# Kernel optimization log

Measured on AMD Instinct MI355X. Metric: run time of the kernel, lower is better.

Reference implementation:

```python
import jax, jax.numpy as jnp
import numpy as np

N = 8192
IN_F = 256
OUT_F = 128
ALPHA = 0.2  # LeakyReLU negative slope
NEG = -1e12


def setup_inputs() -> dict:
    key = jax.random.key(0)
    k1, k2, k3, k4, k5, k6 = jax.random.split(key, 6)
    inp = jax.random.normal(k1, (N, IN_F), dtype=jnp.float32)
    adj = jax.random.randint(k2, (N, N), 0, 2, dtype=jnp.int32)
    # xavier_uniform with gain=1.414
    def xavier(k, shape, gain=1.414):
        fan_in, fan_out = shape[0], shape[1]
        bound = gain * np.sqrt(6.0 / (fan_in + fan_out))
        return jax.random.uniform(k, shape, jnp.float32, -bound, bound)
    W = xavier(k3, (IN_F, OUT_F))
    a = xavier(k4, (2 * OUT_F, 1))
    W_2 = xavier(k5, (IN_F, OUT_F))
    a_2 = xavier(k6, (2 * OUT_F, 1))
    return {"inp": inp, "adj": adj, "W": W, "a": a, "W_2": W_2, "a_2": a_2}


def _gat_head(h, a_vec, mask):
    # Equivalent to e[i,j] = leakyrelu(a^T [h_i ; h_j]) without N^2*2F concat:
    # split a into source/destination halves.
    a_src = a_vec[:OUT_F, 0]   # [F]
    a_dst = a_vec[OUT_F:, 0]   # [F]
    e = (h @ a_src)[:, None] + (h @ a_dst)[None, :]        # [N, N]
    e = jnp.where(e > 0, e, ALPHA * e)                      # LeakyReLU
    e = jnp.where(mask, e, NEG)
    att = jax.nn.softmax(e, axis=1)                         # [N, N]
    # dropout omitted (eval mode, training=False)
    return att @ h                                          # [N, F]


def reference(inp, adj, W, a, W_2, a_2):
    h = inp @ W      # [N, F]
    h_2 = inp @ W_2  # [N, F]
    mask = adj > 0   # adj is nonneg ints so adj*adj>0 is the same mask
    h_prime = _gat_head(h, a, mask)
    h_prime_2 = _gat_head(h_2, a_2, mask)
    h_total = h_prime + 0.5 * h_prime_2
    return jax.nn.elu(h_total)  # concat=True
```

## Files before the change

kernel.cpp:

```cpp
#include <hip/hip_runtime.h>
#include <hip/hip_fp16.h>

#define NN 8192
#define INF 256
#define OUTF 128
#define LOG2E 1.44269504088896340736f

typedef float f32x4 __attribute__((ext_vector_type(4)));
typedef float f32x16 __attribute__((ext_vector_type(16)));
typedef __fp16 h16x8 __attribute__((ext_vector_type(8)));
typedef __fp16 h16x4 __attribute__((ext_vector_type(4)));
typedef __fp16 h16x2 __attribute__((ext_vector_type(2)));
typedef int i32x4 __attribute__((ext_vector_type(4)));

__device__ __forceinline__ void gload_lds16(const void* g, void* l) {
  __builtin_amdgcn_global_load_lds(
      (const __attribute__((address_space(1))) unsigned int*)g,
      (__attribute__((address_space(3))) unsigned int*)l, 16, 0, 0);
}

__device__ __forceinline__ unsigned encf(float f) {
  int b = __float_as_int(f);
  return b >= 0 ? ((unsigned)b | 0x80000000u) : ~(unsigned)b;
}
__device__ __forceinline__ float decf(unsigned u) {
  int b = (u & 0x80000000u) ? (int)(u & 0x7FFFFFFFu) : ~(int)u;
  return __int_as_float(b);
}

__global__ __launch_bounds__(256) void k0_wt(const float* __restrict__ W1,
                                             const float* __restrict__ W2,
                                             __fp16* __restrict__ WT,
                                             unsigned* __restrict__ GMu) {
  if (blockIdx.x == 0 && threadIdx.x < 2) GMu[threadIdx.x] = 0u;
  int m = blockIdx.x * 256 + threadIdx.x;
  int h = m >> 12;
  int r = m & 4095;
  int c = r >> 5;
  int kb = (r >> 1) & 15;
  int hh = r & 1;
  const float* W = h ? W2 : W1;
  float v[8];
#pragma unroll
  for (int s = 0; s < 8; ++s) {
    int koff = 4 * hh + (s & 3) + 8 * (s >> 2);
    v[s] = W[(kb * 16 + koff) * OUTF + c];
  }
  union { h16x2 h2[4]; i32x4 q; } u;
  u.h2[0] = __builtin_amdgcn_cvt_pkrtz(v[0], v[1]);
  u.h2[1] = __builtin_amdgcn_cvt_pkrtz(v[2], v[3]);
  u.h2[2] = __builtin_amdgcn_cvt_pkrtz(v[4], v[5]);
  u.h2[3] = __builtin_amdgcn_cvt_pkrtz(v[6], v[7]);
  *(i32x4*)(WT + (size_t)h * 32768 + c * 256 + kb * 16 + hh * 8) = u.q;
}

__global__ __launch_bounds__(128) void k1_h(
    const float* __restrict__ inp, const __fp16* __restrict__ WT,
    const float* __restrict__ a1, const float* __restrict__ a2,
    __fp16* __restrict__ hT2, float* __restrict__ S, float* __restrict__ D,
    unsigned* __restrict__ GMu) {
  __shared__ __align__(16) float hl[2][32][136];
  int tid = threadIdx.x;
  int w = tid >> 6;
  int l = tid & 63;
  int lr = l & 31, g = l >> 5;
  int i0 = blockIdx.x * 32;
  const __fp16* WTh = WT + (size_t)w * 32768;
  f32x16 acc[4];
#pragma unroll
  for (int nf = 0; nf < 4; ++nf)
#pragma unroll
    for (int e = 0; e < 16; ++e) acc[nf][e] = 0.0f;
  const float* ip = inp + (size_t)(i0 + lr) * INF;
#pragma unroll
  for (int kb = 0; kb < 16; ++kb) {
    f32x4 q0 = *(const f32x4*)(ip + kb * 16 + 4 * g);
    f32x4 q1 = *(const f32x4*)(ip + kb * 16 + 8 + 4 * g);
    union { h16x2 h2[4]; h16x8 h8; } ua;
    ua.h2[0] = __builtin_amdgcn_cvt_pkrtz(q0[0], q0[1]);
    ua.h2[1] = __builtin_amdgcn_cvt_pkrtz(q0[2], q0[3]);
    ua.h2[2] = __builtin_amdgcn_cvt_pkrtz(q1[0], q1[1]);
    ua.h2[3] = __builtin_amdgcn_cvt_pkrtz(q1[2], q1[3]);
#pragma unroll
    for (int nf = 0; nf < 4; ++nf) {
      h16x8 b = *(const h16x8*)(WTh + (nf * 32 + lr) * 256 + kb * 16 + g * 8);
      acc[nf] = __builtin_amdgcn_mfma_f32_32x32x16_f16(ua.h8, b, acc[nf], 0, 0, 0);
    }
  }
#pragma unroll
  for (int nf = 0; nf < 4; ++nf)
#pragma unroll
    for (int r = 0; r < 16; ++r) {
      int row = (r & 3) + 8 * (r >> 2) + 4 * g;
      hl[w][row][nf * 32 + lr] = acc[nf][r];
    }
  __syncthreads();
  const float* av = w ? a2 : a1;
  float s = 0.f, d = 0.f;
#pragma unroll
  for (int cc = 0; cc < 64; cc += 4) {
    int c = g * 64 + cc;
    f32x4 hv = *(const f32x4*)&hl[w][lr][c];
    f32x4 as = *(const f32x4*)(av + c);
    f32x4 ad = *(const f32x4*)(av + 128 + c);
    s += hv[0] * as[0] + hv[1] * as[1] + hv[2] * as[2] + hv[3] * as[3];
    d += hv[0] * ad[0] + hv[1] * ad[1] + hv[2] * ad[2] + hv[3] * ad[3];
  }
  s += __shfl_xor(s, 32);
  d += __shfl_xor(d, 32);
  float dl = d * LOG2E;
  if (g == 0) {
    S[(size_t)w * NN + i0 + lr] = s * LOG2E;
    D[(size_t)w * NN + i0 + lr] = dl;
  }
  float dmax = dl;
#pragma unroll
  for (int off = 1; off < 32; off <<= 1) dmax = fmaxf(dmax, __shfl_xor(dmax, off));
  if (l == 0) atomicMax(GMu + w, encf(dmax));
  __fp16* hTh = hT2 + (size_t)w * (NN * OUTF);
#pragma unroll
  for (int it = 0; it < 8; ++it) {
    int id = it * 64 + l;
    int jb = id >> 8;
    int sub = id & 255;
    int nf = sub >> 6, lq = sub & 63;
    int lqr = lq & 31, lqg = lq >> 5;
    float v[8];
#pragma unroll
    for (int s2 = 0; s2 < 8; ++s2) {
      int kloc = 4 * lqg + (s2 & 3) + 8 * (s2 >> 2);
      v[s2] = hl[w][jb * 16 + kloc][nf * 32 + lqr];
    }
    union { h16x2 h2[4]; i32x4 q; } u2;
    u2.h2[0] = __builtin_amdgcn_cvt_pkrtz(v[0], v[1]);
    u2.h2[1] = __builtin_amdgcn_cvt_pkrtz(v[2], v[3]);
    u2.h2[2] = __builtin_amdgcn_cvt_pkrtz(v[4], v[5]);
    u2.h2[3] = __builtin_amdgcn_cvt_pkrtz(v[6], v[7]);
    *(i32x4*)(hTh + (size_t)((i0 >> 4) + jb) * 2048 + sub * 8) = u2.q;
  }
}

__global__ __launch_bounds__(256, 2) void k2_attn(
    const int* __restrict__ adj, const __fp16* __restrict__ hT2,
    const float* __restrict__ S, const float* __restrict__ D,
    const unsigned* __restrict__ GMu, __fp16* __restrict__ NUM,
    float* __restrict__ DEN) {
  __shared__ __align__(16) char smem[32768];
  __shared__ __align__(16) char maskL[10240];
  int tid = threadIdx.x;
  int w = tid >> 6;
  int l = tid & 63;
  int lr = l & 31, g2 = l >> 5;
  int h = w >> 1, rq = w & 1;
  int rb = blockIdx.x >> 3, js = blockIdx.x & 7;
  int i0 = rb * 128;
  int jwin = js * 1024;
  int base = i0 + rq * 64;
  int row0 = base + lr, row1 = base + 32 + lr;
  float gm = decf(GMu[h]);
  float sf0 = S[(size_t)h * NN + row0];
  float sf1 = S[(size_t)h * NN + row1];
  float t0 = sf0 + gm, t1 = sf1 + gm;
  float cn0 = -fmaxf(t0, 0.2f * t0) - 1000.0f;
  float cn1 = -fmaxf(t1, 0.2f * t1) - 1000.0f;
  float Ac0 = sf0 + cn0, Bc0 = 0.2f * sf0 + cn0;
  float Ac1 = sf1 + cn1, Bc1 = 0.2f * sf1 + cn1;
  const float* Dh = D + (size_t)h * NN + jwin + 4 * g2;

  f32x16 acc[2][4];
#pragma unroll
  for (int f = 0; f < 2; ++f)
#pragma unroll
    for (int nf = 0; nf < 4; ++nf)
#pragma unroll
      for (int e = 0; e < 16; ++e) acc[f][nf][e] = 0.0f;
  float dsum0 = 0.f, dsum1 = 0.f;

  auto STAGE = [&](int jstep, int b) {
#pragma unroll
    for (int q = 0; q < 4; ++q) {
      int kk_l = q >> 1, hh = q & 1;
      const __fp16* gs = hT2 + (size_t)hh * (NN * OUTF) +
                         (size_t)(js * 64 + jstep * 2 + kk_l) * 2048 + tid * 8;
      gload_lds16(gs, smem + b * 16384 + q * 4096 + tid * 16);
    }
  };

  struct Chunk { i32x4 v0, v1, v2, v3; };
  auto LOADC = [&](int c, Chunk& R) {
    int u = c & 7, gg = c >> 3;
    const int* ab = adj + (size_t)(i0 + w * 32 + u * 4) * NN + jwin + gg * 256 + l * 4;
    R.v0 = *(const i32x4*)(ab);
    R.v1 = *(const i32x4*)(ab + NN);
    R.v2 = *(const i32x4*)(ab + 2 * NN);
    R.v3 = *(const i32x4*)(ab + 3 * NN);
  };
  auto BALLOT = [&](int c, const Chunk& R) {
    int u = c & 7, gg = c >> 3;
    char* mrow = maskL + (gg & 1) * 5120 + (w * 32 + u * 4) * 40 + l * 8;
#pragma unroll
    for (int rr = 0; rr < 4; ++rr) {
      i32x4 vv = rr == 0 ? R.v0 : rr == 1 ? R.v1 : rr == 2 ? R.v2 : R.v3;
      unsigned long long b0 = __ballot(vv[0] != 0);
      unsigned long long b1 = __ballot(vv[1] != 0);
      unsigned long long b2 = __ballot(vv[2] != 0);
      unsigned long long b3 = __ballot(vv[3] != 0);
      unsigned long long bsel = b0;
      bsel = (l == 1) ? b1 : bsel;
      bsel = (l == 2) ? b2 : bsel;
      bsel = (l == 3) ? b3 : bsel;
      if (l < 4) *(unsigned long long*)(mrow + rr * 40) = bsel;
    }
  };

  auto MASK32 = [&](int slot, int r, int u) -> unsigned {
    const unsigned char* mb = (const unsigned char*)(maskL + slot * 5120 + r * 40 + u);
    unsigned m0 = mb[0], m1 = mb[8], m2 = mb[16], m3 = mb[24];
    return m0 | (m1 << 8) | (m2 << 16) | (m3 << 24);
  };

  const h16x2 ones = {(__fp16)1.0f, (__fp16)1.0f};
  h16x8 P[2][2];

  auto SOFTMAX = [&](int jstep, int slot, int u) {
    unsigned bts0 = MASK32(slot, rq * 64 + lr, u) >> g2;
    unsigned bts1 = MASK32(slot, rq * 64 + 32 + lr, u) >> g2;
#pragma unroll
    for (int kk = 0; kk < 2; ++kk) {
      int kkg = jstep * 2 + kk;
      f32x4 d0 = *(const f32x4*)(Dh + kkg * 16);
      f32x4 d1 = *(const f32x4*)(Dh + kkg * 16 + 8);
#pragma unroll
      for (int f = 0; f < 2; ++f) {
        float Af = f ? Ac1 : Ac0, Bf_ = f ? Bc1 : Bc0;
        unsigned bts = f ? bts1 : bts0;
        float pv[8];
#pragma unroll
        for (int s = 0; s < 8; ++s) {
          float dd = (s < 4) ? d0[s] : d1[s - 4];
          const int bitp = 8 * (s & 3) + 4 * kk + 2 * (s >> 2);
          float uu = fmaxf(Af + dd, fmaf(0.2f, dd, Bf_));
          float bfv = (float)((bts >> bitp) & 1u);
          pv[s] = __builtin_amdgcn_exp2f(fmaf(bfv, 1000.0f, uu));
        }
        union { h16x2 h2[4]; h16x8 h8; } uq;
        uq.h2[0] = __builtin_amdgcn_cvt_pkrtz(pv[0], pv[1]);
        uq.h2[1] = __builtin_amdgcn_cvt_pkrtz(pv[2], pv[3]);
        uq.h2[2] = __builtin_amdgcn_cvt_pkrtz(pv[4], pv[5]);
        uq.h2[3] = __builtin_amdgcn_cvt_pkrtz(pv[6], pv[7]);
        float ds = f ? dsum1 : dsum0;
#if __has_builtin(__builtin_amdgcn_fdot2)
        ds = __builtin_amdgcn_fdot2(uq.h2[0], ones, ds, false);
        ds = __builtin_amdgcn_fdot2(uq.h2[1], ones, ds, false);
        ds = __builtin_amdgcn_fdot2(uq.h2[2], ones, ds, false);
        ds = __builtin_amdgcn_fdot2(uq.h2[3], ones, ds, false);
#else
        ds += ((pv[0] + pv[1]) + (pv[2] + pv[3])) + ((pv[4] + pv[5]) + (pv[6] + pv[7]));
#endif
        if (f) dsum1 = ds; else dsum0 = ds;
        P[f][kk] = uq.h8;
      }
    }
  };

  auto MFMA_STEP = [&](int b) {
#pragma unroll
    for (int kk = 0; kk < 2; ++kk) {
      const char* lb = smem + b * 16384 + (kk * 2 + h) * 4096 + l * 16;
#pragma unroll
      for (int nf = 0; nf < 4; ++nf) {
        h16x8 Bf = *(const h16x8*)(lb + nf * 1024);
        acc[0][nf] = __builtin_amdgcn_mfma_f32_32x32x16_f16(P[0][kk], Bf, acc[0][nf], 0, 0, 0);
        acc[1][nf] = __builtin_amdgcn_mfma_f32_32x32x16_f16(P[1][kk], Bf, acc[1][nf], 0, 0, 0);
      }
    }
  };

  Chunk RA, RB;
#pragma unroll
  for (int c = 0; c < 8; ++c) { Chunk T; LOADC(c, T); BALLOT(c, T); }
  LOADC(8, RA);
  LOADC(9, RB);
  STAGE(0, 0);
  __syncthreads();

  for (int g = 0; g < 4; ++g) {
#pragma unroll
    for (int u = 0; u < 8; ++u) {
      const int jstep = g * 8 + u;
      const int b = u & 1;
      if (jstep < 31) STAGE(jstep + 1, b ^ 1);
      if (g < 3) {
        if (u & 1) { BALLOT(jstep + 8, RB); if (jstep + 10 < 32) LOADC(jstep + 10, RB); }
        else       { BALLOT(jstep + 8, RA); if (jstep + 10 < 32) LOADC(jstep + 10, RA); }
      }
      SOFTMAX(jstep, g & 1, u);
      MFMA_STEP(b);
      __syncthreads();
    }
  }

  dsum0 += __shfl_xor(dsum0, 32);
  dsum1 += __shfl_xor(dsum1, 32);
  if (g2 == 0) {
    DEN[(size_t)(js * 2 + h) * NN + row0] = dsum0;
    DEN[(size_t)(js * 2 + h) * NN + row1] = dsum1;
  }
#pragma unroll
  for (int f = 0; f < 2; ++f) {
    __fp16* nb = NUM + ((size_t)(js * 2 + h) * NN + base + f * 32) * 128 + lr;
#pragma unroll
    for (int nf = 0; nf < 4; ++nf)
#pragma unroll
      for (int r = 0; r < 16; ++r) {
        int crow = (r & 3) + 8 * (r >> 2) + 4 * g2;
        nb[(size_t)crow * 128 + nf * 32] = (__fp16)acc[f][nf][r];
      }
  }
}

__global__ __launch_bounds__(256) void k3_out(const __fp16* __restrict__ NUM,
                                              const float* __restrict__ DEN,
                                              float* __restrict__ out) {
  int gid = blockIdx.x * 256 + threadIdx.x;
  int i = gid >> 5;
  int c4 = (gid & 31) * 4;
  f32x4 n1 = {0.f, 0.f, 0.f, 0.f}, n2 = {0.f, 0.f, 0.f, 0.f};
  float d1 = 0.f, d2 = 0.f;
#pragma unroll
  for (int js = 0; js < 8; ++js) {
    h16x4 a1v = *(const h16x4*)(NUM + ((size_t)(js * 2 + 0) * NN + i) * 128 + c4);
    h16x4 a2v = *(const h16x4*)(NUM + ((size_t)(js * 2 + 1) * NN + i) * 128 + c4);
#pragma unroll
    for (int e = 0; e < 4; ++e) { n1[e] += (float)a1v[e]; n2[e] += (float)a2v[e]; }
    d1 += DEN[(size_t)(js * 2 + 0) * NN + i];
    d2 += DEN[(size_t)(js * 2 + 1) * NN + i];
  }
  float r1 = 1.0f / d1, r2 = 0.5f / d2;
  f32x4 o;
#pragma unroll
  for (int e = 0; e < 4; ++e) {
    float x = n1[e] * r1 + n2[e] * r2;
    o[e] = x > 0.f ? x : (exp2f(x * LOG2E) - 1.0f);
  }
  *(f32x4*)(out + (size_t)i * 128 + c4) = o;
}

extern "C" void kernel_launch(void* const* d_in, const int* in_sizes, int n_in,
                              void* d_out, int out_size, void* d_ws, size_t ws_size,
                              hipStream_t stream) {
  const float* inp = (const float*)d_in[0];
  const int* adj = (const int*)d_in[1];
  const float* W1 = (const float*)d_in[2];
  const float* a1 = (const float*)d_in[3];
  const float* W2 = (const float*)d_in[4];
  const float* a2 = (const float*)d_in[5];
  float* out = (float*)d_out;
  char* ws = (char*)d_ws;
  __fp16* WT = (__fp16*)(ws);
  __fp16* hT2 = (__fp16*)(ws + 131072);
  float* S = (float*)(ws + 4325376);
  float* D = (float*)(ws + 4390912);
  unsigned* GMu = (unsigned*)(ws + 4456448);
  __fp16* NUM = (__fp16*)(ws + 12845312);
  float* DEN = (float*)(ws + 46399744);

  k0_wt<<<dim3(32), dim3(256), 0, stream>>>(W1, W2, WT, GMu);
  k1_h<<<dim3(256), dim3(128), 0, stream>>>(inp, WT, a1, a2, hT2, S, D, GMu);
  k2_attn<<<dim3(512), dim3(256), 0, stream>>>(adj, hT2, S, D, GMu, NUM, DEN);
  k3_out<<<dim3(1024), dim3(256), 0, stream>>>(NUM, DEN, out);
}
```

Before: 117.5 us.

## Halve attention block row tile to 64 rows and raise occupancy to three blocks

Cuts the rows each k2_attn block handles from 128 to 64, so each wave owns one 32-row fragment instead of two. This halves the accumulator registers and mask LDS, lets launch bounds ask for 3 blocks per CU, and doubles the grid to 1024 blocks. The mask ballot pipeline is reworked for the smaller tile. The cost is that each staged hT2 tile now feeds half as many MFMAs, so B-operand reuse per LDS load falls and global traffic for h rises.

```diff
diff --git a/kernel.cpp b/kernel.cpp
--- a/kernel.cpp
+++ b/kernel.cpp
@@ -140,41 +140,37 @@
   }
 }
 
-__global__ __launch_bounds__(256, 2) void k2_attn(
+__global__ __launch_bounds__(256, 3) void k2_attn(
     const int* __restrict__ adj, const __fp16* __restrict__ hT2,
     const float* __restrict__ S, const float* __restrict__ D,
     const unsigned* __restrict__ GMu, __fp16* __restrict__ NUM,
     float* __restrict__ DEN) {
   __shared__ __align__(16) char smem[32768];
-  __shared__ __align__(16) char maskL[10240];
+  __shared__ __align__(16) char maskL[5120];
   int tid = threadIdx.x;
   int w = tid >> 6;
   int l = tid & 63;
   int lr = l & 31, g2 = l >> 5;
   int h = w >> 1, rq = w & 1;
   int rb = blockIdx.x >> 3, js = blockIdx.x & 7;
-  int i0 = rb * 128;
+  int i0 = rb * 64;
   int jwin = js * 1024;
-  int base = i0 + rq * 64;
-  int row0 = base + lr, row1 = base + 32 + lr;
+  int row = i0 + rq * 32 + lr;
   float gm = decf(GMu[h]);
-  float sf0 = S[(size_t)h * NN + row0];
-  float sf1 = S[(size_t)h * NN + row1];
-  float t0 = sf0 + gm, t1 = sf1 + gm;
-  float cn0 = -fmaxf(t0, 0.2f * t0) - 1000.0f;
-  float cn1 = -fmaxf(t1, 0.2f * t1) - 1000.0f;
-  float Ac0 = sf0 + cn0, Bc0 = 0.2f * sf0 + cn0;
-  float Ac1 = sf1 + cn1, Bc1 = 0.2f * sf1 + cn1;
+  float sf = S[(size_t)h * NN + row];
+  float t0 = sf + gm;
+  float cn = -fmaxf(t0, 0.2f * t0) - 1000.0f;
+  float Ac = sf + cn, Bc = 0.2f * sf + cn;
   const float* Dh = D + (size_t)h * NN + jwin + 4 * g2;
 
-  f32x16 acc[2][4];
-#pragma unroll
-  for (int f = 0; f < 2; ++f)
-#pragma unroll
-    for (int nf = 0; nf < 4; ++nf)
-#pragma unroll
-      for (int e = 0; e < 16; ++e) acc[f][nf][e] = 0.0f;
-  float dsum0 = 0.f, dsum1 = 0.f;
+  f32x4 accq[4];
+  f32x16 acc[4];
+#pragma unroll
+  for (int nf = 0; nf < 4; ++nf)
+#pragma unroll
+    for (int e = 0; e < 16; ++e) acc[nf][e] = 0.0f;
+  (void)accq;
+  float dsum = 0.f;
 
   auto STAGE = [&](int jstep, int b) {
 #pragma unroll
@@ -187,17 +183,17 @@
   };
 
   struct Chunk { i32x4 v0, v1, v2, v3; };
-  auto LOADC = [&](int c, Chunk& R) {
-    int u = c & 7, gg = c >> 3;
-    const int* ab = adj + (size_t)(i0 + w * 32 + u * 4) * NN + jwin + gg * 256 + l * 4;
+  auto LOADC = [&](int m, Chunk& R) {
+    int c = m & 3, g = m >> 2;
+    const int* ab = adj + (size_t)(i0 + w * 16 + c * 4) * NN + jwin + g * 256 + l * 4;
     R.v0 = *(const i32x4*)(ab);
     R.v1 = *(const i32x4*)(ab + NN);
     R.v2 = *(const i32x4*)(ab + 2 * NN);
     R.v3 = *(const i32x4*)(ab + 3 * NN);
   };
-  auto BALLOT = [&](int c, const Chunk& R) {
-    int u = c & 7, gg = c >> 3;
-    char* mrow = maskL + (gg & 1) * 5120 + (w * 32 + u * 4) * 40 + l * 8;
+  auto BALLOT = [&](int m, const Chunk& R) {
+    int c = m & 3, g = m >> 2;
+    char* mrow = maskL + (g & 1) * 2560 + (w * 16 + c * 4) * 40 + l * 8;
 #pragma unroll
     for (int rr = 0; rr < 4; ++rr) {
       i32x4 vv = rr == 0 ? R.v0 : rr == 1 ? R.v1 : rr == 2 ? R.v2 : R.v3;
@@ -214,52 +210,44 @@
   };
 
   auto MASK32 = [&](int slot, int r, int u) -> unsigned {
-    const unsigned char* mb = (const unsigned char*)(maskL + slot * 5120 + r * 40 + u);
+    const unsigned char* mb = (const unsigned char*)(maskL + slot * 2560 + r * 40 + u);
     unsigned m0 = mb[0], m1 = mb[8], m2 = mb[16], m3 = mb[24];
     return m0 | (m1 << 8) | (m2 << 16) | (m3 << 24);
   };
 
   const h16x2 ones = {(__fp16)1.0f, (__fp16)1.0f};
-  h16x8 P[2][2];
+  h16x8 P[2];
 
   auto SOFTMAX = [&](int jstep, int slot, int u) {
-    unsigned bts0 = MASK32(slot, rq * 64 + lr, u) >> g2;
-    unsigned bts1 = MASK32(slot, rq * 64 + 32 + lr, u) >> g2;
+    unsigned bts = MASK32(slot, rq * 32 + lr, u) >> g2;
 #pragma unroll
     for (int kk = 0; kk < 2; ++kk) {
       int kkg = jstep * 2 + kk;
       f32x4 d0 = *(const f32x4*)(Dh + kkg * 16);
       f32x4 d1 = *(const f32x4*)(Dh + kkg * 16 + 8);
-#pragma unroll
-      for (int f = 0; f < 2; ++f) {
-        float Af = f ? Ac1 : Ac0, Bf_ = f ? Bc1 : Bc0;
-        unsigned bts = f ? bts1 : bts0;
-        float pv[8];
-#pragma unroll
-        for (int s = 0; s < 8; ++s) {
-          float dd = (s < 4) ? d0[s] : d1[s - 4];
-          const int bitp = 8 * (s & 3) + 4 * kk + 2 * (s >> 2);
-          float uu = fmaxf(Af + dd, fmaf(0.2f, dd, Bf_));
-          float bfv = (float)((bts >> bitp) & 1u);
-          pv[s] = __builtin_amdgcn_exp2f(fmaf(bfv, 1000.0f, uu));
-        }
-        union { h16x2 h2[4]; h16x8 h8; } uq;
-        uq.h2[0] = __builtin_amdgcn_cvt_pkrtz(pv[0], pv[1]);
-        uq.h2[1] = __builtin_amdgcn_cvt_pkrtz(pv[2], pv[3]);
-        uq.h2[2] = __builtin_amdgcn_cvt_pkrtz(pv[4], pv[5]);
-        uq.h2[3] = __builtin_amdgcn_cvt_pkrtz(pv[6], pv[7]);
-        float ds = f ? dsum1 : dsum0;
+      float pv[8];
+#pragma unroll
+      for (int s = 0; s < 8; ++s) {
+        float dd = (s < 4) ? d0[s] : d1[s - 4];
+        const int bitp = 8 * (s & 3) + 4 * kk + 2 * (s >> 2);
+        float uu = fmaxf(Ac + dd, fmaf(0.2f, dd, Bc));
+        float bfv = (float)((bts >> bitp) & 1u);
+        pv[s] = __builtin_amdgcn_exp2f(fmaf(bfv, 1000.0f, uu));
+      }
+      union { h16x2 h2[4]; h16x8 h8; } uq;
+      uq.h2[0] = __builtin_amdgcn_cvt_pkrtz(pv[0], pv[1]);
+      uq.h2[1] = __builtin_amdgcn_cvt_pkrtz(pv[2], pv[3]);
+      uq.h2[2] = __builtin_amdgcn_cvt_pkrtz(pv[4], pv[5]);
+      uq.h2[3] = __builtin_amdgcn_cvt_pkrtz(pv[6], pv[7]);
 #if __has_builtin(__builtin_amdgcn_fdot2)
-        ds = __builtin_amdgcn_fdot2(uq.h2[0], ones, ds, false);
-        ds = __builtin_amdgcn_fdot2(uq.h2[1], ones, ds, false);
-        ds = __builtin_amdgcn_fdot2(uq.h2[2], ones, ds, false);
-        ds = __builtin_amdgcn_fdot2(uq.h2[3], ones, ds, false);
+      dsum = __builtin_amdgcn_fdot2(uq.h2[0], ones, dsum, false);
+      dsum = __builtin_amdgcn_fdot2(uq.h2[1], ones, dsum, false);
+      dsum = __builtin_amdgcn_fdot2(uq.h2[2], ones, dsum, false);
+      dsum = __builtin_amdgcn_fdot2(uq.h2[3], ones, dsum, false);
 #else
-        ds += ((pv[0] + pv[1]) + (pv[2] + pv[3])) + ((pv[4] + pv[5]) + (pv[6] + pv[7]));
+      dsum += ((pv[0] + pv[1]) + (pv[2] + pv[3])) + ((pv[4] + pv[5]) + (pv[6] + pv[7]));
 #endif
-        if (f) dsum1 = ds; else dsum0 = ds;
-        P[f][kk] = uq.h8;
-      }
+      P[kk] = uq.h8;
     }
   };
 
@@ -270,17 +258,18 @@
 #pragma unroll
       for (int nf = 0; nf < 4; ++nf) {
         h16x8 Bf = *(const h16x8*)(lb + nf * 1024);
-        acc[0][nf] = __builtin_amdgcn_mfma_f32_32x32x16_f16(P[0][kk], Bf, acc[0][nf], 0, 0, 0);
-        acc[1][nf] = __builtin_amdgcn_mfma_f32_32x32x16_f16(P[1][kk], Bf, acc[1][nf], 0, 0, 0);
+        acc[nf] = __builtin_amdgcn_mfma_f32_32x32x16_f16(P[kk], Bf, acc[nf], 0, 0, 0);
       }
     }
   };
 
-  Chunk RA, RB;
-#pragma unroll
-  for (int c = 0; c < 8; ++c) { Chunk T; LOADC(c, T); BALLOT(c, T); }
-  LOADC(8, RA);
-  LOADC(9, RB);
+  Chunk R0, R1;
+  LOADC(0, R0);
+  LOADC(1, R1);
+  BALLOT(0, R0); LOADC(2, R0);
+  BALLOT(1, R1); LOADC(3, R1);
+  BALLOT(2, R0); LOADC(4, R0);
+  BALLOT(3, R1); LOADC(5, R1);
   STAGE(0, 0);
   __syncthreads();
 
@@ -288,11 +277,13 @@
 #pragma unroll
     for (int u = 0; u < 8; ++u) {
       const int jstep = g * 8 + u;
-      const int b = u & 1;
+      const int b = jstep & 1;
       if (jstep < 31) STAGE(jstep + 1, b ^ 1);
-      if (g < 3) {
-        if (u & 1) { BALLOT(jstep + 8, RB); if (jstep + 10 < 32) LOADC(jstep + 10, RB); }
-        else       { BALLOT(jstep + 8, RA); if (jstep + 10 < 32) LOADC(jstep + 10, RA); }
+      if (g < 3 && !(u & 1)) {
+        const int p = u >> 1;
+        const int m = (g + 1) * 4 + p;
+        if (p & 1) { BALLOT(m, R1); if (m + 2 < 16) LOADC(m + 2, R1); }
+        else       { BALLOT(m, R0); if (m + 2 < 16) LOADC(m + 2, R0); }
       }
       SOFTMAX(jstep, g & 1, u);
       MFMA_STEP(b);
@@ -300,23 +291,16 @@
     }
   }
 
-  dsum0 += __shfl_xor(dsum0, 32);
-  dsum1 += __shfl_xor(dsum1, 32);
-  if (g2 == 0) {
-    DEN[(size_t)(js * 2 + h) * NN + row0] = dsum0;
-    DEN[(size_t)(js * 2 + h) * NN + row1] = dsum1;
-  }
-#pragma unroll
-  for (int f = 0; f < 2; ++f) {
-    __fp16* nb = NUM + ((size_t)(js * 2 + h) * NN + base + f * 32) * 128 + lr;
-#pragma unroll
-    for (int nf = 0; nf < 4; ++nf)
-#pragma unroll
-      for (int r = 0; r < 16; ++r) {
-        int crow = (r & 3) + 8 * (r >> 2) + 4 * g2;
-        nb[(size_t)crow * 128 + nf * 32] = (__fp16)acc[f][nf][r];
-      }
-  }
+  dsum += __shfl_xor(dsum, 32);
+  if (g2 == 0) DEN[(size_t)(js * 2 + h) * NN + row] = dsum;
+  __fp16* nb = NUM + ((size_t)(js * 2 + h) * NN + i0 + rq * 32) * 128 + lr;
+#pragma unroll
+  for (int nf = 0; nf < 4; ++nf)
+#pragma unroll
+    for (int r = 0; r < 16; ++r) {
+      int crow = (r & 3) + 8 * (r >> 2) + 4 * g2;
+      nb[(size_t)crow * 128 + nf * 32] = (__fp16)acc[nf][r];
+    }
 }
 
 __global__ __launch_bounds__(256) void k3_out(const __fp16* __restrict__ NUM,
@@ -367,6 +351,6 @@
 
   k0_wt<<<dim3(32), dim3(256), 0, stream>>>(W1, W2, WT, GMu);
   k1_h<<<dim3(256), dim3(128), 0, stream>>>(inp, WT, a1, a2, hT2, S, D, GMu);
-  k2_attn<<<dim3(512), dim3(256), 0, stream>>>(adj, hT2, S, D, GMu, NUM, DEN);
+  k2_attn<<<dim3(1024), dim3(256), 0, stream>>>(adj, hT2, S, D, GMu, NUM, DEN);
   k3_out<<<dim3(1024), dim3(256), 0, stream>>>(NUM, DEN, out);
 }
```

After: 132.0 us. 1.12x slower.

## Fuse output kernel into attention via in-block split-K reduction with per-wave pipelines

Applied to the files above, without the earlier changes.

Restructures the attention kernel so each 512-thread block owns 32 rows and its 8 waves each cover a 1024-column window for both heads. The partial numerators and denominators are reduced through LDS inside the block, and the normalisation plus ELU is applied in place. This removes the separate k3_out kernel and the fp16 NUM/DEN round trip through global memory. Each wave now stages its own hT2 tiles and uses waitcnt instead of block-wide barriers in the main loop. The trade-offs are large LDS use (about 150KB), only 256 blocks, and a reduction epilogue.

```diff
diff --git a/kernel.cpp b/kernel.cpp
--- a/kernel.cpp
+++ b/kernel.cpp
@@ -9,7 +9,6 @@
 typedef float f32x4 __attribute__((ext_vector_type(4)));
 typedef float f32x16 __attribute__((ext_vector_type(16)));
 typedef __fp16 h16x8 __attribute__((ext_vector_type(8)));
-typedef __fp16 h16x4 __attribute__((ext_vector_type(4)));
 typedef __fp16 h16x2 __attribute__((ext_vector_type(2)));
 typedef int i32x4 __attribute__((ext_vector_type(4)));
 
@@ -140,64 +139,60 @@
   }
 }
 
-__global__ __launch_bounds__(256, 2) void k2_attn(
+__global__ __launch_bounds__(512, 2) void k2_attn(
     const int* __restrict__ adj, const __fp16* __restrict__ hT2,
     const float* __restrict__ S, const float* __restrict__ D,
-    const unsigned* __restrict__ GMu, __fp16* __restrict__ NUM,
-    float* __restrict__ DEN) {
-  __shared__ __align__(16) char smem[32768];
-  __shared__ __align__(16) char maskL[10240];
+    const unsigned* __restrict__ GMu, float* __restrict__ out) {
+  __shared__ __align__(16) char smem[153856];
   int tid = threadIdx.x;
   int w = tid >> 6;
   int l = tid & 63;
   int lr = l & 31, g2 = l >> 5;
-  int h = w >> 1, rq = w & 1;
-  int rb = blockIdx.x >> 3, js = blockIdx.x & 7;
-  int i0 = rb * 128;
-  int jwin = js * 1024;
-  int base = i0 + rq * 64;
-  int row0 = base + lr, row1 = base + 32 + lr;
-  float gm = decf(GMu[h]);
-  float sf0 = S[(size_t)h * NN + row0];
-  float sf1 = S[(size_t)h * NN + row1];
-  float t0 = sf0 + gm, t1 = sf1 + gm;
+  int i0 = blockIdx.x * 32;
+  int jwin = w * 1024;
+  char* wavebase = smem + w * 16384;
+  char* maskw = smem + 131072 + w * 2560;
+
+  float gm0 = decf(GMu[0]), gm1 = decf(GMu[1]);
+  float sf0 = S[i0 + lr];
+  float sf1 = S[NN + i0 + lr];
+  float t0 = sf0 + gm0, t1 = sf1 + gm1;
   float cn0 = -fmaxf(t0, 0.2f * t0) - 1000.0f;
   float cn1 = -fmaxf(t1, 0.2f * t1) - 1000.0f;
   float Ac0 = sf0 + cn0, Bc0 = 0.2f * sf0 + cn0;
   float Ac1 = sf1 + cn1, Bc1 = 0.2f * sf1 + cn1;
-  const float* Dh = D + (size_t)h * NN + jwin + 4 * g2;
+  const float* D0 = D + jwin;
+  const float* D1 = D + NN + jwin;
 
   f32x16 acc[2][4];
 #pragma unroll
-  for (int f = 0; f < 2; ++f)
+  for (int h = 0; h < 2; ++h)
 #pragma unroll
     for (int nf = 0; nf < 4; ++nf)
 #pragma unroll
-      for (int e = 0; e < 16; ++e) acc[f][nf][e] = 0.0f;
+      for (int e = 0; e < 16; ++e) acc[h][nf][e] = 0.0f;
   float dsum0 = 0.f, dsum1 = 0.f;
 
-  auto STAGE = [&](int jstep, int b) {
-#pragma unroll
-    for (int q = 0; q < 4; ++q) {
-      int kk_l = q >> 1, hh = q & 1;
-      const __fp16* gs = hT2 + (size_t)hh * (NN * OUTF) +
-                         (size_t)(js * 64 + jstep * 2 + kk_l) * 2048 + tid * 8;
-      gload_lds16(gs, smem + b * 16384 + q * 4096 + tid * 16);
+  auto STAGE = [&](int t2, int b) {
+#pragma unroll
+    for (int q = 0; q < 8; ++q) {
+      int h = q >> 2, part = q & 3;
+      const __fp16* gs = hT2 + (size_t)h * (NN * OUTF) +
+                         (size_t)(w * 64 + t2) * 2048 + (part * 64 + l) * 8;
+      gload_lds16(gs, wavebase + b * 8192 + h * 4096 + part * 1024 + l * 16);
     }
   };
 
   struct Chunk { i32x4 v0, v1, v2, v3; };
-  auto LOADC = [&](int c, Chunk& R) {
-    int u = c & 7, gg = c >> 3;
-    const int* ab = adj + (size_t)(i0 + w * 32 + u * 4) * NN + jwin + gg * 256 + l * 4;
+  auto LOADC = [&](int gg, int pp, Chunk& R) {
+    const int* ab = adj + (size_t)(i0 + pp * 4) * NN + jwin + gg * 256 + l * 4;
     R.v0 = *(const i32x4*)(ab);
     R.v1 = *(const i32x4*)(ab + NN);
     R.v2 = *(const i32x4*)(ab + 2 * NN);
     R.v3 = *(const i32x4*)(ab + 3 * NN);
   };
-  auto BALLOT = [&](int c, const Chunk& R) {
-    int u = c & 7, gg = c >> 3;
-    char* mrow = maskL + (gg & 1) * 5120 + (w * 32 + u * 4) * 40 + l * 8;
+  auto BALLOT = [&](int gg, int pp, const Chunk& R) {
+    char* mrow = maskw + (gg & 1) * 1280 + (pp * 4) * 40 + l * 8;
 #pragma unroll
     for (int rr = 0; rr < 4; ++rr) {
       i32x4 vv = rr == 0 ? R.v0 : rr == 1 ? R.v1 : rr == 2 ? R.v2 : R.v3;
@@ -212,138 +207,163 @@
       if (l < 4) *(unsigned long long*)(mrow + rr * 40) = bsel;
     }
   };
-
-  auto MASK32 = [&](int slot, int r, int u) -> unsigned {
-    const unsigned char* mb = (const unsigned char*)(maskL + slot * 5120 + r * 40 + u);
-    unsigned m0 = mb[0], m1 = mb[8], m2 = mb[16], m3 = mb[24];
-    return m0 | (m1 << 8) | (m2 << 16) | (m3 << 24);
+  auto MASK16 = [&](int slot, int u) -> unsigned {
+    const unsigned char* mb =
+        (const unsigned char*)(maskw + slot * 1280 + lr * 40 + (u >> 1));
+    unsigned n0 = (mb[0] >> ((u & 1) * 4)) & 0xFu;
+    unsigned n1 = (mb[8] >> ((u & 1) * 4)) & 0xFu;
+    unsigned n2 = (mb[16] >> ((u & 1) * 4)) & 0xFu;
+    unsigned n3 = (mb[24] >> ((u & 1) * 4)) & 0xFu;
+    return n0 | (n1 << 4) | (n2 << 8) | (n3 << 12);
   };
 
   const h16x2 ones = {(__fp16)1.0f, (__fp16)1.0f};
-  h16x8 P[2][2];
-
-  auto SOFTMAX = [&](int jstep, int slot, int u) {
-    unsigned bts0 = MASK32(slot, rq * 64 + lr, u) >> g2;
-    unsigned bts1 = MASK32(slot, rq * 64 + 32 + lr, u) >> g2;
-#pragma unroll
-    for (int kk = 0; kk < 2; ++kk) {
-      int kkg = jstep * 2 + kk;
-      f32x4 d0 = *(const f32x4*)(Dh + kkg * 16);
-      f32x4 d1 = *(const f32x4*)(Dh + kkg * 16 + 8);
-#pragma unroll
-      for (int f = 0; f < 2; ++f) {
-        float Af = f ? Ac1 : Ac0, Bf_ = f ? Bc1 : Bc0;
-        unsigned bts = f ? bts1 : bts0;
-        float pv[8];
-#pragma unroll
-        for (int s = 0; s < 8; ++s) {
-          float dd = (s < 4) ? d0[s] : d1[s - 4];
-          const int bitp = 8 * (s & 3) + 4 * kk + 2 * (s >> 2);
-          float uu = fmaxf(Af + dd, fmaf(0.2f, dd, Bf_));
-          float bfv = (float)((bts >> bitp) & 1u);
-          pv[s] = __builtin_amdgcn_exp2f(fmaf(bfv, 1000.0f, uu));
-        }
-        union { h16x2 h2[4]; h16x8 h8; } uq;
-        uq.h2[0] = __builtin_amdgcn_cvt_pkrtz(pv[0], pv[1]);
-        uq.h2[1] = __builtin_amdgcn_cvt_pkrtz(pv[2], pv[3]);
-        uq.h2[2] = __builtin_amdgcn_cvt_pkrtz(pv[4], pv[5]);
-        uq.h2[3] = __builtin_amdgcn_cvt_pkrtz(pv[6], pv[7]);
-        float ds = f ? dsum1 : dsum0;
+  h16x8 P[2];
+
+  auto SOFTMAX = [&](int t, int slot, int u) {
+    unsigned bts = MASK16(slot, u) >> g2;
+#pragma unroll
+    for (int h = 0; h < 2; ++h) {
+      const float* Dh = h ? D1 : D0;
+      float Af = h ? Ac1 : Ac0, Bf_ = h ? Bc1 : Bc0;
+      f32x4 d0 = *(const f32x4*)(Dh + t * 16 + 4 * g2);
+      f32x4 d1 = *(const f32x4*)(Dh + t * 16 + 4 * g2 + 8);
+      float pv[8];
+#pragma unroll
+      for (int s = 0; s < 8; ++s) {
+        float dd = (s < 4) ? d0[s] : d1[s - 4];
+        const int bitp = 4 * (s & 3) + 2 * (s >> 2);
+        float uu = fmaxf(Af + dd, fmaf(0.2f, dd, Bf_));
+        float bfv = (float)((bts >> bitp) & 1u);
+        pv[s] = __builtin_amdgcn_exp2f(fmaf(bfv, 1000.0f, uu));
+      }
+      union { h16x2 h2[4]; h16x8 h8; } uq;
+      uq.h2[0] = __builtin_amdgcn_cvt_pkrtz(pv[0], pv[1]);
+      uq.h2[1] = __builtin_amdgcn_cvt_pkrtz(pv[2], pv[3]);
+      uq.h2[2] = __builtin_amdgcn_cvt_pkrtz(pv[4], pv[5]);
+      uq.h2[3] = __builtin_amdgcn_cvt_pkrtz(pv[6], pv[7]);
+      float ds = h ? dsum1 : dsum0;
 #if __has_builtin(__builtin_amdgcn_fdot2)
-        ds = __builtin_amdgcn_fdot2(uq.h2[0], ones, ds, false);
-        ds = __builtin_amdgcn_fdot2(uq.h2[1], ones, ds, false);
-        ds = __builtin_amdgcn_fdot2(uq.h2[2], ones, ds, false);
-        ds = __builtin_amdgcn_fdot2(uq.h2[3], ones, ds, false);
+      ds = __builtin_amdgcn_fdot2(uq.h2[0], ones, ds, false);
+      ds = __builtin_amdgcn_fdot2(uq.h2[1], ones, ds, false);
+      ds = __builtin_amdgcn_fdot2(uq.h2[2], ones, ds, false);
+      ds = __builtin_amdgcn_fdot2(uq.h2[3], ones, ds, false);
 #else
-        ds += ((pv[0] + pv[1]) + (pv[2] + pv[3])) + ((pv[4] + pv[5]) + (pv[6] + pv[7]));
+      ds += ((pv[0] + pv[1]) + (pv[2] + pv[3])) + ((pv[4] + pv[5]) + (pv[6] + pv[7]));
 #endif
-        if (f) dsum1 = ds; else dsum0 = ds;
-        P[f][kk] = uq.h8;
-      }
+      if (h) dsum1 = ds; else dsum0 = ds;
+      P[h] = uq.h8;
     }
   };
 
   auto MFMA_STEP = [&](int b) {
 #pragma unroll
-    for (int kk = 0; kk < 2; ++kk) {
-      const char* lb = smem + b * 16384 + (kk * 2 + h) * 4096 + l * 16;
+    for (int h = 0; h < 2; ++h) {
+      const char* lb = wavebase + b * 8192 + h * 4096 + l * 16;
 #pragma unroll
       for (int nf = 0; nf < 4; ++nf) {
         h16x8 Bf = *(const h16x8*)(lb + nf * 1024);
-        acc[0][nf] = __builtin_amdgcn_mfma_f32_32x32x16_f16(P[0][kk], Bf, acc[0][nf], 0, 0, 0);
-        acc[1][nf] = __builtin_amdgcn_mfma_f32_32x32x16_f16(P[1][kk], Bf, acc[1][nf], 0, 0, 0);
+        acc[h][nf] = __builtin_amdgcn_mfma_f32_32x32x16_f16(P[h], Bf, acc[h][nf], 0, 0, 0);
       }
     }
   };
 
-  Chunk RA, RB;
-#pragma unroll
-  for (int c = 0; c < 8; ++c) { Chunk T; LOADC(c, T); BALLOT(c, T); }
-  LOADC(8, RA);
-  LOADC(9, RB);
+  Chunk R0, R1;
+  LOADC(0, 0, R0);
+  LOADC(0, 1, R1);
+  BALLOT(0, 0, R0); LOADC(0, 2, R0);
+  BALLOT(0, 1, R1); LOADC(0, 3, R1);
+  BALLOT(0, 2, R0); LOADC(0, 4, R0);
+  BALLOT(0, 3, R1); LOADC(0, 5, R1);
+  BALLOT(0, 4, R0); LOADC(0, 6, R0);
+  BALLOT(0, 5, R1); LOADC(0, 7, R1);
+  BALLOT(0, 6, R0); LOADC(1, 0, R0);
+  BALLOT(0, 7, R1); LOADC(1, 1, R1);
   STAGE(0, 0);
-  __syncthreads();
+  STAGE(1, 1);
+  asm volatile("s_waitcnt vmcnt(0) lgkmcnt(0)" ::: "memory");
+  __builtin_amdgcn_sched_barrier(0);
 
   for (int g = 0; g < 4; ++g) {
 #pragma unroll
-    for (int u = 0; u < 8; ++u) {
-      const int jstep = g * 8 + u;
-      const int b = u & 1;
-      if (jstep < 31) STAGE(jstep + 1, b ^ 1);
-      if (g < 3) {
-        if (u & 1) { BALLOT(jstep + 8, RB); if (jstep + 10 < 32) LOADC(jstep + 10, RB); }
-        else       { BALLOT(jstep + 8, RA); if (jstep + 10 < 32) LOADC(jstep + 10, RA); }
+    for (int u = 0; u < 16; ++u) {
+      const int t = g * 16 + u;
+      const int b = t & 1;
+      if (t < 63) STAGE(t + 1, b ^ 1);
+      __builtin_amdgcn_sched_barrier(0);
+      if ((u & 1) == 0 && g < 3) {
+        const int p = u >> 1;
+        if (p & 1) {
+          BALLOT(g + 1, p, R1);
+          if (p < 6) LOADC(g + 1, p + 2, R1);
+          else if (g < 2) LOADC(g + 2, p - 6, R1);
+        } else {
+          BALLOT(g + 1, p, R0);
+          if (p < 6) LOADC(g + 1, p + 2, R0);
+          else if (g < 2) LOADC(g + 2, p - 6, R0);
+        }
       }
-      SOFTMAX(jstep, g & 1, u);
+      __builtin_amdgcn_sched_barrier(0);
+      SOFTMAX(t, g & 1, u);
+      asm volatile("s_waitcnt vmcnt(16)" ::: "memory");
+      __builtin_amdgcn_sched_barrier(0);
       MFMA_STEP(b);
-      __syncthreads();
     }
   }
 
   dsum0 += __shfl_xor(dsum0, 32);
   dsum1 += __shfl_xor(dsum1, 32);
-  if (g2 == 0) {
-    DEN[(size_t)(js * 2 + h) * NN + row0] = dsum0;
-    DEN[(size_t)(js * 2 + h) * NN + row1] = dsum1;
-  }
-#pragma unroll
-  for (int f = 0; f < 2; ++f) {
-    __fp16* nb = NUM + ((size_t)(js * 2 + h) * NN + base + f * 32) * 128 + lr;
-#pragma unroll
-    for (int nf = 0; nf < 4; ++nf)
-#pragma unroll
-      for (int r = 0; r < 16; ++r) {
-        int crow = (r & 3) + 8 * (r >> 2) + 4 * g2;
-        nb[(size_t)crow * 128 + nf * 32] = (__fp16)acc[f][nf][r];
-      }
-  }
-}
-
-__global__ __launch_bounds__(256) void k3_out(const __fp16* __restrict__ NUM,
-                                              const float* __restrict__ DEN,
-                                              float* __restrict__ out) {
-  int gid = blockIdx.x * 256 + threadIdx.x;
-  int i = gid >> 5;
-  int c4 = (gid & 31) * 4;
-  f32x4 n1 = {0.f, 0.f, 0.f, 0.f}, n2 = {0.f, 0.f, 0.f, 0.f};
-  float d1 = 0.f, d2 = 0.f;
-#pragma unroll
-  for (int js = 0; js < 8; ++js) {
-    h16x4 a1v = *(const h16x4*)(NUM + ((size_t)(js * 2 + 0) * NN + i) * 128 + c4);
-    h16x4 a2v = *(const h16x4*)(NUM + ((size_t)(js * 2 + 1) * NN + i) * 128 + c4);
-#pragma unroll
-    for (int e = 0; e < 4; ++e) { n1[e] += (float)a1v[e]; n2[e] += (float)a2v[e]; }
-    d1 += DEN[(size_t)(js * 2 + 0) * NN + i];
-    d2 += DEN[(size_t)(js * 2 + 1) * NN + i];
-  }
-  float r1 = 1.0f / d1, r2 = 0.5f / d2;
-  f32x4 o;
-#pragma unroll
-  for (int e = 0; e < 4; ++e) {
-    float x = n1[e] * r1 + n2[e] * r2;
-    o[e] = x > 0.f ? x : (exp2f(x * LOG2E) - 1.0f);
-  }
-  *(f32x4*)(out + (size_t)i * 128 + c4) = o;
+  float* dsums = (float*)(smem + 151552);
+  if (l < 32) {
+    dsums[w * 64 + l] = dsum0;
+    dsums[w * 64 + 32 + l] = dsum1;
+  }
+  __syncthreads();
+  float* Rg = (float*)(void*)(smem) + (size_t)(w & 3) * 8192;
+  if (w < 4) {
+#pragma unroll
+    for (int h = 0; h < 2; ++h)
+#pragma unroll
+      for (int nf = 0; nf < 4; ++nf)
+#pragma unroll
+        for (int r = 0; r < 16; ++r)
+          Rg[((h * 4 + nf) * 16 + r) * 64 + l] = acc[h][nf][r];
+  }
+  __syncthreads();
+  if (w >= 4) {
+#pragma unroll
+    for (int h = 0; h < 2; ++h)
+#pragma unroll
+      for (int nf = 0; nf < 4; ++nf)
+#pragma unroll
+        for (int r = 0; r < 16; ++r)
+          Rg[((h * 4 + nf) * 16 + r) * 64 + l] += acc[h][nf][r];
+  }
+  float* den2 = (float*)(smem + 153600);
+  if (w == 0) {
+    float dl2 = 0.f;
+#pragma unroll
+    for (int ww = 0; ww < 8; ++ww) dl2 += dsums[ww * 64 + l];
+    den2[l] = dl2;
+  }
+  __syncthreads();
+  const float* R0p = (const float*)(void*)smem;
+#pragma unroll
+  for (int k = 0; k < 8; ++k) {
+    int combo = w * 8 + k;
+    int nf = combo >> 4, r = combo & 15;
+    int crow = (r & 3) + 8 * (r >> 2) + 4 * g2;
+    float a0 = 0.f, a1 = 0.f;
+#pragma unroll
+    for (int rg = 0; rg < 4; ++rg) {
+      a0 += R0p[rg * 8192 + ((0 * 4 + nf) * 16 + r) * 64 + l];
+      a1 += R0p[rg * 8192 + ((1 * 4 + nf) * 16 + r) * 64 + l];
+    }
+    float d0 = den2[crow], d1 = den2[32 + crow];
+    float x = a0 / d0 + 0.5f * (a1 / d1);
+    float o = x > 0.f ? x : (__builtin_amdgcn_exp2f(x * LOG2E) - 1.0f);
+    out[(size_t)(i0 + crow) * 128 + nf * 32 + lr] = o;
+  }
 }
 
 extern "C" void kernel_launch(void* const* d_in, const int* in_sizes, int n_in,
@@ -362,11 +382,8 @@
   float* S = (float*)(ws + 4325376);
   float* D = (float*)(ws + 4390912);
   unsigned* GMu = (unsigned*)(ws + 4456448);
-  __fp16* NUM = (__fp16*)(ws + 12845312);
-  float* DEN = (float*)(ws + 46399744);
 
   k0_wt<<<dim3(32), dim3(256), 0, stream>>>(W1, W2, WT, GMu);
   k1_h<<<dim3(256), dim3(128), 0, stream>>>(inp, WT, a1, a2, hT2, S, D, GMu);
-  k2_attn<<<dim3(512), dim3(256), 0, stream>>>(adj, hT2, S, D, GMu, NUM, DEN);
-  k3_out<<<dim3(1024), dim3(256), 0, stream>>>(NUM, DEN, out);
-}
+  k2_attn<<<dim3(256), dim3(512), 0, stream>>>(adj, hT2, S, D, GMu, out);
+}
```

Result: slower. 228.0 us (+94.0%).
